# Optimization experiments

Hardware: AMD Instinct MI355X
Metric: run time of the kernel (lower is better)

The kernel has to match this reference:

```python
import jax, jax.numpy as jnp
import numpy as np
import math

B, T, E, H, L, FF = 8, 512, 1024, 16, 4, 4096
D = E // H
LN_EPS = 1e-5


def _layernorm(x, g, b):
    mu = jnp.mean(x, axis=-1, keepdims=True)
    var = jnp.mean((x - mu) ** 2, axis=-1, keepdims=True)
    return (x - mu) * jax.lax.rsqrt(var + LN_EPS) * g + b


def setup_inputs() -> dict:
    key = jax.random.key(0)
    ks = jax.random.split(key, 16)
    s = 0.02
    return {
        "src": jax.random.normal(ks[0], (B, T, E), jnp.float32),
        "in_proj_w": jax.random.normal(ks[1], (L, 3 * E, E), jnp.float32) * s,
        "in_proj_b": jax.random.normal(ks[2], (L, 3 * E), jnp.float32) * s,
        "out_w": jax.random.normal(ks[3], (L, E, E), jnp.float32) * s,
        "out_b": jnp.zeros((L, E), jnp.float32),
        "ff1_w": jax.random.normal(ks[4], (L, FF, E), jnp.float32) * s,
        "ff1_b": jnp.zeros((L, FF), jnp.float32),
        "ff2_w": jax.random.normal(ks[5], (L, E, FF), jnp.float32) * s,
        "ff2_b": jnp.zeros((L, E), jnp.float32),
        "ln1_g": jnp.ones((L, E), jnp.float32),
        "ln1_b": jnp.zeros((L, E), jnp.float32),
        "ln2_g": jnp.ones((L, E), jnp.float32),
        "ln2_b": jnp.zeros((L, E), jnp.float32),
        "head_w": jax.random.normal(ks[6], (1, E), jnp.float32) * s,
        "head_b": jnp.zeros((1,), jnp.float32),
    }


def reference(src, in_proj_w, in_proj_b, out_w, out_b, ff1_w, ff1_b,
              ff2_w, ff2_b, ln1_g, ln1_b, ln2_g, ln2_b, head_w, head_b):
    b, t, e = src.shape
    # --- PositionalEncoding (faithful to batch_first bug: pe indexed by batch dim) ---
    pos = jnp.arange(b, dtype=jnp.float32)[:, None]            # [B,1]
    div = jnp.exp(jnp.arange(0, e, 2, dtype=jnp.float32) * (-math.log(10000.0) / e))
    pe = jnp.zeros((b, e), jnp.float32)
    pe = pe.at[:, 0::2].set(jnp.sin(pos * div)).at[:, 1::2].set(jnp.cos(pos * div))
    x = src + pe[:, None, :]                                   # broadcast over seq

    # --- Gaussian bias, shared across layers (Tq == Tk == T) ---
    dist = jnp.arange(t)[:, None] - jnp.arange(t)[None, :]
    gb = jnp.exp(-(dist.astype(jnp.float32) ** 2) / (2.0 * (t / 4.0) ** 2))  # [T,T]

    for l in range(L):
        qkv = x @ in_proj_w[l].T + in_proj_b[l]                # [B,T,3E]
        q, k, v = jnp.split(qkv, 3, axis=-1)
        q = q.reshape(b, t, H, D).transpose(0, 2, 1, 3)        # [B,H,T,D]
        k = k.reshape(b, t, H, D).transpose(0, 2, 1, 3)
        v = v.reshape(b, t, H, D).transpose(0, 2, 1, 3)
        scores = jnp.einsum("bhqd,bhkd->bhqk", q, k) / math.sqrt(D)
        w = jax.nn.softmax(scores, axis=-1)                    # [B,H,Tq,Tk]
        w = w * gb[None, None]
        w = w / (jnp.sum(w, axis=-1, keepdims=True) + 1e-5)
        o = jnp.einsum("bhqk,bhkd->bhqd", w, v)
        o = o.transpose(0, 2, 1, 3).reshape(b, t, e)
        o = o @ out_w[l].T + out_b[l]
        x = _layernorm(x + o, ln1_g[l], ln1_b[l])              # post-norm
        ff = jax.nn.relu(x @ ff1_w[l].T + ff1_b[l]) @ ff2_w[l].T + ff2_b[l]
        x = _layernorm(x + ff, ln2_g[l], ln2_b[l])

    last = x[:, -1, :]                                         # [B,E]
    return last @ head_w.T + head_b                            # [B,1]
```

## Files before the change

kernel.cpp:

```cpp
#include <hip/hip_runtime.h>

typedef unsigned short u16;
typedef __attribute__((ext_vector_type(4))) float v4f;
typedef __attribute__((ext_vector_type(8))) short v8bf;

__device__ inline u16 f2bf(float f){
  union { float f; unsigned u; } v; v.f = f;
  unsigned r = (v.u + 0x7FFFu + ((v.u >> 16) & 1u)) >> 16;
  return (u16)r;
}
__device__ inline float bf2f(u16 u){
  union { unsigned u; float f; } v; v.u = ((unsigned)u) << 16;
  return v.f;
}

#define GLD_LDS16(gp, lp) \
  __builtin_amdgcn_global_load_lds((const __attribute__((address_space(1))) void*)(gp), \
                                   (__attribute__((address_space(3))) void*)(lp), 16, 0, 0)
#define VMCNT(n) asm volatile("s_waitcnt vmcnt(" #n ")" ::: "memory")
#define LGKM0 do { asm volatile("s_waitcnt lgkmcnt(0)" ::: "memory"); \
                   __builtin_amdgcn_sched_barrier(0); } while (0)

template<int FUSE>
__global__ __launch_bounds__(512, 2) void gemm9(
    const u16* __restrict__ A, const u16* __restrict__ W,
    const float* __restrict__ bias, void* __restrict__ C,
    int N, int K, int Kc, int gx, int gy)
{
  __shared__ u16 smem[65536];
  const int tid = threadIdx.x, lane = tid & 63, wid = tid >> 6;
  const int wm = wid >> 2, wn = wid & 3;

  const int nwg = gridDim.x, bid = blockIdx.x;
  const int swz = (bid & 7) * (nwg >> 3) + (bid >> 3);
  const int gxy = gx * gy;
  const int bz = swz / gxy;
  const int rem = swz - bz * gxy;
  const int by = rem / gx;
  const int bx = rem - by * gx;
  const int k0 = bz * Kc;
  const int NT = Kc >> 6;

  const int arow = (wid >> 1) * 16 + (lane & 15);
  const int akk  = (wid & 1) * 32 + ((lane >> 4) << 3);
  const u16* gA = A + (size_t)(by * 256 + arow) * K + k0 + akk;
  const u16* gB = W + (size_t)(bx * 256 + arow) * K + k0 + akk;
  u16* ldst = smem + tid * 8;

  auto stageA = [&](int t, int h) {
    u16* d = ldst + (t & 1) * 32768 + h * 8192;
    const u16* s = gA + (size_t)(h * 128) * K + t * 64;
    GLD_LDS16(s, d);
    GLD_LDS16(s + (size_t)64 * K, d + 4096);
  };
  auto stageB = [&](int t, int h) {
    u16* d = ldst + (t & 1) * 32768 + (2 + h) * 8192;
    const u16* s = gB + (size_t)(h * 128) * K + t * 64;
    GLD_LDS16(s, d);
    GLD_LDS16(s + (size_t)64 * K, d + 4096);
  };

  v4f acc[8][4];
  #pragma unroll
  for (int i = 0; i < 8; ++i)
    #pragma unroll
    for (int j = 0; j < 4; ++j) acc[i][j] = (v4f){0.f, 0.f, 0.f, 0.f};

  stageA(0, 0); stageA(0, 1); stageB(0, 0); stageB(0, 1);
  if (NT > 1) { stageA(1, 0); stageA(1, 1); VMCNT(4); } else { VMCNT(0); }
  __builtin_amdgcn_s_barrier();

  const u16* rdA = smem + wm * 8192 + lane * 8;
  const u16* rdB = smem + 16384 + (wn >> 1) * 8192 + lane * 8;
  const int jb = (wn & 1) * 4;

  v8bf aq[4][2], bq[4][2];

#define MFMA_CL(QI, NLO)                                                        \
  do {                                                                          \
    __builtin_amdgcn_s_setprio(1);                                              \
    _Pragma("unroll") for (int m = 0; m < 4; ++m)                               \
      _Pragma("unroll") for (int n = NLO; n < NLO + 2; ++n)                     \
        _Pragma("unroll") for (int kk = 0; kk < 2; ++kk)                        \
          acc[(QI)*4 + m][n] = __builtin_amdgcn_mfma_f32_16x16x32_bf16(         \
              aq[m][kk], bq[n][kk], acc[(QI)*4 + m][n], 0, 0, 0);               \
    __builtin_amdgcn_s_setprio(0);                                              \
  } while (0)

  for (int t = 0; t < NT; ++t) {
    const int bufo = (t & 1) * 32768;
    __builtin_amdgcn_sched_barrier(0);
    #pragma unroll
    for (int m = 0; m < 4; ++m)
      #pragma unroll
      for (int kk = 0; kk < 2; ++kk)
        aq[m][kk] = *(const v8bf*)(rdA + bufo + (m * 2 + kk) * 512);
    #pragma unroll
    for (int n = 0; n < 2; ++n)
      #pragma unroll
      for (int kk = 0; kk < 2; ++kk)
        bq[n][kk] = *(const v8bf*)(rdB + bufo + ((jb + n) * 2 + kk) * 512);
    if (t + 1 < NT) stageB(t + 1, 0);
    MFMA_CL(0, 0);
    #pragma unroll
    for (int n = 2; n < 4; ++n)
      #pragma unroll
      for (int kk = 0; kk < 2; ++kk)
        bq[n][kk] = *(const v8bf*)(rdB + bufo + ((jb + n) * 2 + kk) * 512);
    if (t + 1 < NT) stageB(t + 1, 1);
    MFMA_CL(0, 2);
    __builtin_amdgcn_s_barrier();
    __builtin_amdgcn_sched_barrier(0);
    #pragma unroll
    for (int m = 0; m < 4; ++m)
      #pragma unroll
      for (int kk = 0; kk < 2; ++kk)
        aq[m][kk] = *(const v8bf*)(rdA + bufo + ((4 + m) * 2 + kk) * 512);
    if (t + 2 < NT) stageA(t + 2, 0);
    MFMA_CL(1, 2);
    __builtin_amdgcn_s_barrier();
    __builtin_amdgcn_sched_barrier(0);
    if (t + 2 < NT) stageA(t + 2, 1);
    MFMA_CL(1, 0);
    if (t < NT - 2) { VMCNT(4); } else if (t == NT - 2) { VMCNT(0); }
    __builtin_amdgcn_s_barrier();
  }
#undef MFMA_CL

  const int cn0 = bx * 256 + wn * 64 + (lane & 15);
  const int rm0 = by * 256 + wm * 128 + ((lane >> 4) << 2);
  if (FUSE == 2) {
    u16* Cp = (u16*)C + (size_t)bz * 4096 * N;
    #pragma unroll
    for (int i = 0; i < 8; ++i)
      #pragma unroll
      for (int r = 0; r < 4; ++r) {
        size_t ro = (size_t)(rm0 + i * 16 + r) * N + cn0;
        #pragma unroll
        for (int j = 0; j < 4; ++j) Cp[ro + j * 16] = f2bf(acc[i][j][r]);
      }
  } else {
    float bv[4];
    #pragma unroll
    for (int j = 0; j < 4; ++j) bv[j] = bias[cn0 + j * 16];
    u16* Cp = (u16*)C;
    #pragma unroll
    for (int i = 0; i < 8; ++i)
      #pragma unroll
      for (int r = 0; r < 4; ++r) {
        size_t ro = (size_t)(rm0 + i * 16 + r) * N + cn0;
        #pragma unroll
        for (int j = 0; j < 4; ++j) {
          float v = acc[i][j][r] + bv[j];
          if (FUSE == 1) v = fmaxf(v, 0.f);
          Cp[ro + j * 16] = f2bf(v);
        }
      }
  }
}

__global__ __launch_bounds__(256, 2) void attn_f(const u16* __restrict__ qkv,
                                                 u16* __restrict__ o)
{
  __shared__ u16 Kf[2][4096];
  __shared__ u16 Vt[2][4096];
  __shared__ u16 wbuf[64 * 72];
  const int tid = threadIdx.x, lane = tid & 63, wid = tid >> 6;
  const int grp = lane >> 4, li = lane & 15;
  const int bh = blockIdx.y, b = bh >> 4, h = bh & 15;
  const int q0 = blockIdx.x * 64;
  const u16* Qg = qkv + (size_t)b * 512 * 3072 + h * 64;
  const u16* Kg = Qg + 1024;
  const u16* Vg = Qg + 2048;

  const size_t qrow = (size_t)(q0 + wid * 16 + li) * 3072;
  v8bf qa0 = *(const v8bf*)(Qg + qrow + grp * 8);
  v8bf qa1 = *(const v8bf*)(Qg + qrow + 32 + grp * 8);

  const u16* kga = Kg + (size_t)(wid * 16 + li) * 3072 + grp * 8;
  auto k_stage = [&](int kt, int buf) {
    #pragma unroll
    for (int s = 0; s < 2; ++s)
      GLD_LDS16(kga + (size_t)kt * 64 * 3072 + s * 32, &Kf[buf][(wid * 2 + s) * 512]);
  };
  auto v_load = [&](int kt, int x) -> v8bf {
    int u = x * 256 + tid, kk = u >> 3, d0 = (u & 7) * 8;
    return *(const v8bf*)(Vg + (size_t)(kt * 64 + kk) * 3072 + d0);
  };
  auto vt_write = [&](int buf, int x, v8bf v) {
    int u = x * 256 + tid, kk = u >> 3, d0 = (u & 7) * 8;
    int kg = (kk >> 3) & 3, kks = kk >> 5, jb2 = (kk & 7) * 2;
    #pragma unroll
    for (int i = 0; i < 8; ++i) {
      int d = d0 + i;
      int byte = (((d >> 4) * 2 + kks) * 1024 + ((d & 15) + 16 * kg) * 16 + jb2)
                 ^ (((d >> 4) & 3) << 5);
      *(u16*)((char*)&Vt[buf][0] + byte) = (u16)v[i];
    }
  };

  v4f oacc[4];
  #pragma unroll
  for (int nt = 0; nt < 4; ++nt) oacc[nt] = (v4f){0.f, 0.f, 0.f, 0.f};
  float mreg[4] = {-1e30f, -1e30f, -1e30f, -1e30f};
  float sg[4] = {0.f, 0.f, 0.f, 0.f};
  float fqv[4];
  #pragma unroll
  for (int j = 0; j < 4; ++j) fqv[j] = (float)(q0 + wid * 16 + grp * 4 + j);

  v8bf vst[2][2];
  k_stage(0, 0);
  k_stage(1, 1);
  vst[0][0] = v_load(0, 0); vst[0][1] = v_load(0, 1);
  VMCNT(0);
  vt_write(0, 0, vst[0][0]); vt_write(0, 1, vst[0][1]);
  vst[1][0] = v_load(1, 0); vst[1][1] = v_load(1, 1);
  LGKM0;
  __builtin_amdgcn_s_barrier();

  const float GC = 3.0517578125e-05f;

  #pragma unroll
  for (int t = 0; t < 8; ++t) {
    const int cur = t & 1;
    v8bf bq0[4], bq1[4];
    #pragma unroll
    for (int nb = 0; nb < 4; ++nb) {
      bq0[nb] = *(const v8bf*)&Kf[cur][(nb * 2 + 0) * 512 + lane * 8];
      bq1[nb] = *(const v8bf*)&Kf[cur][(nb * 2 + 1) * 512 + lane * 8];
    }
    v4f pa[4];
    #pragma unroll
    for (int nb = 0; nb < 4; ++nb) {
      v4f z = (v4f){0.f, 0.f, 0.f, 0.f};
      z = __builtin_amdgcn_mfma_f32_16x16x32_bf16(qa0, bq0[nb], z, 0, 0, 0);
      pa[nb] = __builtin_amdgcn_mfma_f32_16x16x32_bf16(qa1, bq1[nb], z, 0, 0, 0);
    }
    if (t < 7) {
      __builtin_amdgcn_s_barrier();
      __builtin_amdgcn_sched_barrier(0);
      if (t + 2 < 8) k_stage(t + 2, cur);
      if (t < 6) { VMCNT(2); } else { VMCNT(0); }
      vt_write((t + 1) & 1, 0, vst[(t + 1) & 1][0]);
      vt_write((t + 1) & 1, 1, vst[(t + 1) & 1][1]);
      if (t + 2 < 8) { vst[t & 1][0] = v_load(t + 2, 0); vst[t & 1][1] = v_load(t + 2, 1); }
    }
    #pragma unroll
    for (int nb = 0; nb < 4; ++nb) {
      const float fk = (float)(t * 64 + nb * 16 + li);
      #pragma unroll
      for (int j = 0; j < 4; ++j) {
        float d = fqv[j] - fk;
        pa[nb][j] = pa[nb][j] * 0.125f - d * d * GC;
      }
    }
    #pragma unroll
    for (int j = 0; j < 4; ++j) {
      float tmax = fmaxf(fmaxf(pa[0][j], pa[1][j]), fmaxf(pa[2][j], pa[3][j]));
      tmax = fmaxf(tmax, __shfl_xor(tmax, 1));
      tmax = fmaxf(tmax, __shfl_xor(tmax, 2));
      tmax = fmaxf(tmax, __shfl_xor(tmax, 4));
      tmax = fmaxf(tmax, __shfl_xor(tmax, 8));
      float mn = fmaxf(mreg[j], tmax);
      float sc = __expf(mreg[j] - mn);
      mreg[j] = mn;
      float rs = 0.f;
      #pragma unroll
      for (int nb = 0; nb < 4; ++nb) {
        float e = __expf(pa[nb][j] - mn);
        pa[nb][j] = e;
        rs += e;
      }
      rs += __shfl_xor(rs, 1); rs += __shfl_xor(rs, 2);
      rs += __shfl_xor(rs, 4); rs += __shfl_xor(rs, 8);
      sg[j] = sg[j] * sc + rs;
      #pragma unroll
      for (int nt = 0; nt < 4; ++nt) oacc[nt][j] *= sc;
    }
    #pragma unroll
    for (int j = 0; j < 4; ++j) {
      const int row = wid * 16 + grp * 4 + j;
      #pragma unroll
      for (int nb = 0; nb < 4; ++nb)
        wbuf[row * 72 + ((nb * 16 + li) ^ (grp << 3))] = f2bf(pa[nb][j]);
    }
    const int swr = ((li >> 2) & 3) << 3;
    v8bf af0 = *(const v8bf*)&wbuf[(wid * 16 + li) * 72 + ((0 * 32 + grp * 8) ^ swr)];
    v8bf af1 = *(const v8bf*)&wbuf[(wid * 16 + li) * 72 + ((1 * 32 + grp * 8) ^ swr)];
    #pragma unroll
    for (int nt = 0; nt < 4; ++nt) {
      v8bf bv0 = *(const v8bf*)((char*)&Vt[cur][0] + ((((nt * 2 + 0) * 1024) + lane * 16) ^ ((nt & 3) << 5)));
      v8bf bv1 = *(const v8bf*)((char*)&Vt[cur][0] + ((((nt * 2 + 1) * 1024) + lane * 16) ^ ((nt & 3) << 5)));
      oacc[nt] = __builtin_amdgcn_mfma_f32_16x16x32_bf16(af0, bv0, oacc[nt], 0, 0, 0);
      oacc[nt] = __builtin_amdgcn_mfma_f32_16x16x32_bf16(af1, bv1, oacc[nt], 0, 0, 0);
    }
    if (t < 7) {
      if (t < 6) { VMCNT(2); } else { VMCNT(0); }
      LGKM0;
      __builtin_amdgcn_s_barrier();
      __builtin_amdgcn_sched_barrier(0);
    }
  }

  float rin[4];
  #pragma unroll
  for (int j = 0; j < 4; ++j) rin[j] = 1.f / sg[j];
  const size_t obase = (size_t)(b * 512 + q0 + wid * 16 + grp * 4) * 1024 + h * 64;
  #pragma unroll
  for (int nt = 0; nt < 4; ++nt)
    #pragma unroll
    for (int j = 0; j < 4; ++j)
      o[obase + (size_t)j * 1024 + nt * 16 + li] = f2bf(oacc[nt][j] * rin[j]);
}

__global__ __launch_bounds__(256) void ln_res4_k(
    const float* __restrict__ x, const u16* __restrict__ part,
    const float* __restrict__ bias, const float* __restrict__ g,
    const float* __restrict__ beta, float* __restrict__ y, u16* __restrict__ yb)
{
  const int row = blockIdx.x, tid = threadIdx.x;
  const size_t base = (size_t)row * 1024 + tid * 4;
  const size_t MN = 4096ull * 1024;
  float4 xv = *(const float4*)(x + base);
  const int e = tid * 4;
  float4 bb = *(const float4*)(bias + e);
  float v0 = xv.x + bb.x, v1 = xv.y + bb.y, v2 = xv.z + bb.z, v3 = xv.w + bb.w;
  #pragma unroll
  for (int q = 0; q < 4; ++q) {
    ushort4 pv = *(const ushort4*)(part + q * MN + base);
    v0 += bf2f(pv.x); v1 += bf2f(pv.y); v2 += bf2f(pv.z); v3 += bf2f(pv.w);
  }
  float s = v0 + v1 + v2 + v3;
  float q2 = v0*v0 + v1*v1 + v2*v2 + v3*v3;
  #pragma unroll
  for (int m = 1; m < 64; m <<= 1) { s += __shfl_xor(s, m); q2 += __shfl_xor(q2, m); }
  __shared__ float ls[4], lq[4];
  if ((tid & 63) == 0) { ls[tid >> 6] = s; lq[tid >> 6] = q2; }
  __syncthreads();
  s = ls[0] + ls[1] + ls[2] + ls[3];
  q2 = lq[0] + lq[1] + lq[2] + lq[3];
  const float mu = s * (1.f / 1024.f);
  const float var = q2 * (1.f / 1024.f) - mu * mu;
  const float rs = rsqrtf(var + 1e-5f);
  float4 gv = *(const float4*)(g + e);
  float4 be = *(const float4*)(beta + e);
  float o0 = (v0 - mu) * rs * gv.x + be.x;
  float o1 = (v1 - mu) * rs * gv.y + be.y;
  float o2 = (v2 - mu) * rs * gv.z + be.z;
  float o3 = (v3 - mu) * rs * gv.w + be.w;
  *(float4*)(y + base) = make_float4(o0, o1, o2, o3);
  ushort4 ob; ob.x = f2bf(o0); ob.y = f2bf(o1); ob.z = f2bf(o2); ob.w = f2bf(o3);
  *(ushort4*)(yb + base) = ob;
}

__global__ __launch_bounds__(256) void pe_add_k(const float* __restrict__ src,
    float* __restrict__ xf, u16* __restrict__ xb)
{
  const int idx = blockIdx.x * 256 + threadIdx.x;
  const int e = idx & 1023;
  const int b = idx >> 19;
  float freq = __expf((float)(e >> 1) * (-18.420680743952367f * (1.f / 1024.f)));
  float ang = (float)b * freq;
  float pe = (e & 1) ? cosf(ang) : sinf(ang);
  float v = src[idx] + pe;
  xf[idx] = v;
  xb[idx] = f2bf(v);
}

__global__ __launch_bounds__(256) void cvt4_k(const float* __restrict__ s0,
    const float* __restrict__ s1, const float* __restrict__ s2,
    const float* __restrict__ s3, u16* __restrict__ dst)
{
  int i = blockIdx.x * 256 + threadIdx.x;
  const float* s; size_t off;
  if (i < 786432)       { s = s0; off = (size_t)i; }
  else if (i < 1048576) { s = s1; off = (size_t)i - 786432; }
  else if (i < 2097152) { s = s2; off = (size_t)i - 1048576; }
  else                  { s = s3; off = (size_t)i - 2097152; }
  float4 v = ((const float4*)s)[off];
  ushort4 ov; ov.x = f2bf(v.x); ov.y = f2bf(v.y); ov.z = f2bf(v.z); ov.w = f2bf(v.w);
  ((ushort4*)dst)[i] = ov;
}

__global__ __launch_bounds__(256) void head_k(const float* __restrict__ xf,
    const float* __restrict__ hw, const float* __restrict__ hb, float* __restrict__ out)
{
  const int b = blockIdx.x, tid = threadIdx.x;
  const float4 xv = ((const float4*)(xf + ((size_t)b * 512 + 511) * 1024))[tid];
  const float4 wv = ((const float4*)hw)[tid];
  float s = xv.x * wv.x + xv.y * wv.y + xv.z * wv.z + xv.w * wv.w;
  #pragma unroll
  for (int m = 1; m < 64; m <<= 1) s += __shfl_xor(s, m);
  __shared__ float ls[4];
  if ((tid & 63) == 0) ls[tid >> 6] = s;
  __syncthreads();
  if (tid == 0) out[b] = ls[0] + ls[1] + ls[2] + ls[3] + hb[0];
}

extern "C" void kernel_launch(void* const* d_in, const int* in_sizes, int n_in,
                              void* d_out, int out_size, void* d_ws, size_t ws_size,
                              hipStream_t stream)
{
  const float* src  = (const float*)d_in[0];
  const float* ipw  = (const float*)d_in[1];
  const float* ipb  = (const float*)d_in[2];
  const float* outw = (const float*)d_in[3];
  const float* outb = (const float*)d_in[4];
  const float* f1w  = (const float*)d_in[5];
  const float* f1b  = (const float*)d_in[6];
  const float* f2w  = (const float*)d_in[7];
  const float* f2b  = (const float*)d_in[8];
  const float* l1g  = (const float*)d_in[9];
  const float* l1b  = (const float*)d_in[10];
  const float* l2g  = (const float*)d_in[11];
  const float* l2b  = (const float*)d_in[12];
  const float* hw   = (const float*)d_in[13];
  const float* hb   = (const float*)d_in[14];

  char* p = (char*)d_ws;
  auto take = [&](size_t bytes) { char* r = p; p += (bytes + 255) & ~(size_t)255; return r; };
  float* xf   = (float*)take(4096ull * 1024 * 4);
  u16*   xb   = (u16*)  take(4096ull * 1024 * 2);
  u16*   slA  = (u16*)  take(4096ull * 4096 * 2);
  u16*   ob   = (u16*)  take(4096ull * 1024 * 2);
  u16*   pf   = (u16*)  take(4ull * 4096 * 1024 * 2);
  u16*   wc   = (u16*)  take(12582912ull * 2);

  u16* qkvb = slA;
  u16* f1o  = slA;

  pe_add_k<<<16384, 256, 0, stream>>>(src, xf, xb);

  for (int l = 0; l < 4; ++l) {
    cvt4_k<<<12288, 256, 0, stream>>>(ipw + (size_t)l * 3145728,
                                      outw + (size_t)l * 1048576,
                                      f1w + (size_t)l * 4194304,
                                      f2w + (size_t)l * 4194304, wc);
    gemm9<0><<<192, 512, 0, stream>>>(xb, wc, ipb + l * 3072, qkvb, 3072, 1024, 1024, 12, 16);
    attn_f<<<dim3(8, 128), 256, 0, stream>>>(qkvb, ob);
    gemm9<2><<<256, 512, 0, stream>>>(ob, wc + 3145728, nullptr, pf, 1024, 1024, 256, 4, 16);
    ln_res4_k<<<4096, 256, 0, stream>>>(xf, pf, outb + l * 1024, l1g + l * 1024, l1b + l * 1024, xf, xb);
    gemm9<1><<<256, 512, 0, stream>>>(xb, wc + 4194304, f1b + l * 4096, f1o, 4096, 1024, 1024, 16, 16);
    gemm9<2><<<256, 512, 0, stream>>>(f1o, wc + 8388608, nullptr, pf, 1024, 4096, 1024, 4, 16);
    ln_res4_k<<<4096, 256, 0, stream>>>(xf, pf, f2b + l * 1024, l2g + l * 1024, l2b + l * 1024, xf, xb);
  }
  head_k<<<8, 256, 0, stream>>>(xf, hw, hb, (float*)d_out);
}
```

Measured before the change: 889.0 us.

## Drop fp32 residual stream, use exp2 softmax with lazy rescale, vectorize PE add

The fp32 residual copy is removed: layernorm, the positional-encoding add and the head now read and write only the bf16 activations. This cuts memory traffic in the layernorm and PE kernels, at the cost of accumulating the residual in bf16 across layers. The attention softmax folds log2(e) into the score and Gaussian scale constants so it can use exp2, and it skips the running-max rescale while the new tile max stays within a threshold of the stored max. The PE kernel is vectorized to four elements per thread and uses fast sin/cos.

```diff
diff --git a/kernel.cpp b/kernel.cpp
--- a/kernel.cpp
+++ b/kernel.cpp
@@ -218,7 +218,8 @@
   LGKM0;
   __builtin_amdgcn_s_barrier();
 
-  const float GC = 3.0517578125e-05f;
+  const float SC2 = 0.18033688011112042f;
+  const float GC2 = 4.4027559280058695e-05f;
 
   #pragma unroll
   for (int t = 0; t < 8; ++t) {
@@ -251,7 +252,7 @@
       #pragma unroll
       for (int j = 0; j < 4; ++j) {
         float d = fqv[j] - fk;
-        pa[nb][j] = pa[nb][j] * 0.125f - d * d * GC;
+        pa[nb][j] = pa[nb][j] * SC2 - d * d * GC2;
       }
     }
     #pragma unroll
@@ -261,21 +262,24 @@
       tmax = fmaxf(tmax, __shfl_xor(tmax, 2));
       tmax = fmaxf(tmax, __shfl_xor(tmax, 4));
       tmax = fmaxf(tmax, __shfl_xor(tmax, 8));
-      float mn = fmaxf(mreg[j], tmax);
-      float sc = __expf(mreg[j] - mn);
-      mreg[j] = mn;
+      if (!__all(tmax <= mreg[j] + 11.0f)) {
+        float mn = fmaxf(mreg[j], tmax);
+        float sc = exp2f(mreg[j] - mn);
+        mreg[j] = mn;
+        sg[j] *= sc;
+        #pragma unroll
+        for (int nt = 0; nt < 4; ++nt) oacc[nt][j] *= sc;
+      }
       float rs = 0.f;
       #pragma unroll
       for (int nb = 0; nb < 4; ++nb) {
-        float e = __expf(pa[nb][j] - mn);
+        float e = exp2f(pa[nb][j] - mreg[j]);
         pa[nb][j] = e;
         rs += e;
       }
       rs += __shfl_xor(rs, 1); rs += __shfl_xor(rs, 2);
       rs += __shfl_xor(rs, 4); rs += __shfl_xor(rs, 8);
-      sg[j] = sg[j] * sc + rs;
-      #pragma unroll
-      for (int nt = 0; nt < 4; ++nt) oacc[nt][j] *= sc;
+      sg[j] += rs;
     }
     #pragma unroll
     for (int j = 0; j < 4; ++j) {
@@ -314,17 +318,18 @@
 }
 
 __global__ __launch_bounds__(256) void ln_res4_k(
-    const float* __restrict__ x, const u16* __restrict__ part,
+    const u16* __restrict__ x, const u16* __restrict__ part,
     const float* __restrict__ bias, const float* __restrict__ g,
-    const float* __restrict__ beta, float* __restrict__ y, u16* __restrict__ yb)
+    const float* __restrict__ beta, u16* __restrict__ yb)
 {
   const int row = blockIdx.x, tid = threadIdx.x;
   const size_t base = (size_t)row * 1024 + tid * 4;
   const size_t MN = 4096ull * 1024;
-  float4 xv = *(const float4*)(x + base);
+  ushort4 xv = *(const ushort4*)(x + base);
   const int e = tid * 4;
   float4 bb = *(const float4*)(bias + e);
-  float v0 = xv.x + bb.x, v1 = xv.y + bb.y, v2 = xv.z + bb.z, v3 = xv.w + bb.w;
+  float v0 = bf2f(xv.x) + bb.x, v1 = bf2f(xv.y) + bb.y;
+  float v2 = bf2f(xv.z) + bb.z, v3 = bf2f(xv.w) + bb.w;
   #pragma unroll
   for (int q = 0; q < 4; ++q) {
     ushort4 pv = *(const ushort4*)(part + q * MN + base);
@@ -348,23 +353,28 @@
   float o1 = (v1 - mu) * rs * gv.y + be.y;
   float o2 = (v2 - mu) * rs * gv.z + be.z;
   float o3 = (v3 - mu) * rs * gv.w + be.w;
-  *(float4*)(y + base) = make_float4(o0, o1, o2, o3);
   ushort4 ob; ob.x = f2bf(o0); ob.y = f2bf(o1); ob.z = f2bf(o2); ob.w = f2bf(o3);
   *(ushort4*)(yb + base) = ob;
 }
 
 __global__ __launch_bounds__(256) void pe_add_k(const float* __restrict__ src,
-    float* __restrict__ xf, u16* __restrict__ xb)
-{
-  const int idx = blockIdx.x * 256 + threadIdx.x;
-  const int e = idx & 1023;
-  const int b = idx >> 19;
-  float freq = __expf((float)(e >> 1) * (-18.420680743952367f * (1.f / 1024.f)));
-  float ang = (float)b * freq;
-  float pe = (e & 1) ? cosf(ang) : sinf(ang);
-  float v = src[idx] + pe;
-  xf[idx] = v;
-  xb[idx] = f2bf(v);
+    u16* __restrict__ xb)
+{
+  const int u = blockIdx.x * 256 + threadIdx.x;
+  const int e4 = (u & 255) * 4;
+  const int b = u >> 17;
+  const float C = -18.420680743952367f * (1.f / 1024.f);
+  float4 sv = ((const float4*)src)[u];
+  float fb = (float)b;
+  float fr0 = __expf((float)(e4 >> 1) * C);
+  float fr1 = __expf((float)((e4 >> 1) + 1) * C);
+  float a0 = fb * fr0, a1 = fb * fr1;
+  ushort4 ov;
+  ov.x = f2bf(sv.x + __sinf(a0));
+  ov.y = f2bf(sv.y + __cosf(a0));
+  ov.z = f2bf(sv.z + __sinf(a1));
+  ov.w = f2bf(sv.w + __cosf(a1));
+  ((ushort4*)xb)[u] = ov;
 }
 
 __global__ __launch_bounds__(256) void cvt4_k(const float* __restrict__ s0,
@@ -382,13 +392,13 @@
   ((ushort4*)dst)[i] = ov;
 }
 
-__global__ __launch_bounds__(256) void head_k(const float* __restrict__ xf,
+__global__ __launch_bounds__(256) void head_k(const u16* __restrict__ xb,
     const float* __restrict__ hw, const float* __restrict__ hb, float* __restrict__ out)
 {
   const int b = blockIdx.x, tid = threadIdx.x;
-  const float4 xv = ((const float4*)(xf + ((size_t)b * 512 + 511) * 1024))[tid];
+  const ushort4 xv = ((const ushort4*)(xb + ((size_t)b * 512 + 511) * 1024))[tid];
   const float4 wv = ((const float4*)hw)[tid];
-  float s = xv.x * wv.x + xv.y * wv.y + xv.z * wv.z + xv.w * wv.w;
+  float s = bf2f(xv.x) * wv.x + bf2f(xv.y) * wv.y + bf2f(xv.z) * wv.z + bf2f(xv.w) * wv.w;
   #pragma unroll
   for (int m = 1; m < 64; m <<= 1) s += __shfl_xor(s, m);
   __shared__ float ls[4];
@@ -419,7 +429,6 @@
 
   char* p = (char*)d_ws;
   auto take = [&](size_t bytes) { char* r = p; p += (bytes + 255) & ~(size_t)255; return r; };
-  float* xf   = (float*)take(4096ull * 1024 * 4);
   u16*   xb   = (u16*)  take(4096ull * 1024 * 2);
   u16*   slA  = (u16*)  take(4096ull * 4096 * 2);
   u16*   ob   = (u16*)  take(4096ull * 1024 * 2);
@@ -429,7 +438,7 @@
   u16* qkvb = slA;
   u16* f1o  = slA;
 
-  pe_add_k<<<16384, 256, 0, stream>>>(src, xf, xb);
+  pe_add_k<<<4096, 256, 0, stream>>>(src, xb);
 
   for (int l = 0; l < 4; ++l) {
     cvt4_k<<<12288, 256, 0, stream>>>(ipw + (size_t)l * 3145728,
@@ -439,10 +448,10 @@
     gemm9<0><<<192, 512, 0, stream>>>(xb, wc, ipb + l * 3072, qkvb, 3072, 1024, 1024, 12, 16);
     attn_f<<<dim3(8, 128), 256, 0, stream>>>(qkvb, ob);
     gemm9<2><<<256, 512, 0, stream>>>(ob, wc + 3145728, nullptr, pf, 1024, 1024, 256, 4, 16);
-    ln_res4_k<<<4096, 256, 0, stream>>>(xf, pf, outb + l * 1024, l1g + l * 1024, l1b + l * 1024, xf, xb);
+    ln_res4_k<<<4096, 256, 0, stream>>>(xb, pf, outb + l * 1024, l1g + l * 1024, l1b + l * 1024, xb);
     gemm9<1><<<256, 512, 0, stream>>>(xb, wc + 4194304, f1b + l * 4096, f1o, 4096, 1024, 1024, 16, 16);
     gemm9<2><<<256, 512, 0, stream>>>(f1o, wc + 8388608, nullptr, pf, 1024, 4096, 1024, 4, 16);
-    ln_res4_k<<<4096, 256, 0, stream>>>(xf, pf, f2b + l * 1024, l2g + l * 1024, l2b + l * 1024, xf, xb);
+    ln_res4_k<<<4096, 256, 0, stream>>>(xb, pf, f2b + l * 1024, l2g + l * 1024, l2b + l * 1024, xb);
   }
-  head_k<<<8, 256, 0, stream>>>(xf, hw, hb, (float*)d_out);
-}
+  head_k<<<8, 256, 0, stream>>>(xb, hw, hb, (float*)d_out);
+}
```

After: 866.2 us. 2.6% less time.
